# Performance work log

Measured on AMD Instinct MI355X. Metric: run time of the kernel, lower is better.

Reference implementation:

```python
import jax, jax.numpy as jnp
import numpy as np

NUM_HEADS = 8
NUM_POINTS = 4


def setup_inputs() -> dict:
    key = jax.random.key(0)
    ks = jax.random.split(key, 8)
    B, N, C, H, W = 8, 8192, 256, 128, 128
    HP2 = NUM_HEADS * NUM_POINTS * 2
    HP = NUM_HEADS * NUM_POINTS
    query = jax.random.normal(ks[0], (B, N, C), jnp.float32)
    reference_points = jax.random.uniform(ks[1], (B, N, 2), dtype=jnp.float32)
    value = jax.random.normal(ks[2], (B, C, H, W), jnp.float32)
    # learned params (offset gen is zero-init in the original; use small random
    W_off = jax.random.normal(ks[3], (C, HP2), jnp.float32) * 0.02
    b_off = jnp.zeros((HP2,), jnp.float32)
    W_attn = jax.random.normal(ks[4], (C, HP), jnp.float32) * (1.0 / np.sqrt(C))
    b_attn = jnp.zeros((HP,), jnp.float32)
    W_out = jax.random.normal(ks[5], (C, C), jnp.float32) * (1.0 / np.sqrt(C))
    b_out = jnp.zeros((C,), jnp.float32)
    return dict(query=query, reference_points=reference_points, value=value,
                W_off=W_off, b_off=b_off, W_attn=W_attn, b_attn=b_attn,
                W_out=W_out, b_out=b_out, H=H, W=W)


def reference(query, reference_points, value, W_off, b_off, W_attn, b_attn,
              W_out, b_out, H, W):
    B, N, C = query.shape
    Hh, P = NUM_HEADS, NUM_POINTS
    D = C // Hh

    offset = (query @ W_off + b_off).reshape(B, N, Hh, P, 2)
    attn = jax.nn.softmax((query @ W_attn + b_attn).reshape(B, N, Hh, P), axis=-1)

    # sampling locations in grid_sample convention: (x, y) in [-1, 1]
    ref = reference_points * 2.0 - 1.0
    loc = ref[:, :, None, None, :] + offset  # (B, N, Hh, P, 2)

    # value -> (B, Hh, H*W, D)
    val = value.reshape(B, Hh, D, H, W).transpose(0, 1, 3, 4, 2).reshape(B, Hh, H * W, D)

    # align_corners=False pixel coordinates
    x = (loc[..., 0] + 1.0) * (W * 0.5) - 0.5  # (B, N, Hh, P)
    y = (loc[..., 1] + 1.0) * (H * 0.5) - 0.5
    x0f = jnp.floor(x); y0f = jnp.floor(y)
    wx1 = x - x0f; wy1 = y - y0f
    x0 = x0f.astype(jnp.int32); y0 = y0f.astype(jnp.int32)
    x1 = x0 + 1; y1 = y0 + 1

    def gather(ix, iy, w):
        # bilinear corner gather with zero padding (mask out-of-bounds)
        valid = (ix >= 0) & (ix < W) & (iy >= 0) & (iy < H)
        idx = jnp.clip(iy, 0, H - 1) * W + jnp.clip(ix, 0, W - 1)  # (B,N,Hh,P)
        idx_t = idx.transpose(0, 2, 1, 3).reshape(B, Hh, N * P)
        g = jnp.take_along_axis(val, idx_t[..., None], axis=2)  # (B,Hh,N*P,D)
        g = g.reshape(B, Hh, N, P, D).transpose(0, 2, 1, 3, 4)  # (B,N,Hh,P,D)
        return g * (w * valid)[..., None]

    sampled = (gather(x0, y0, (1 - wx1) * (1 - wy1))
               + gather(x1, y0, wx1 * (1 - wy1))
               + gather(x0, y1, (1 - wx1) * wy1)
               + gather(x1, y1, wx1 * wy1))  # (B,N,Hh,P,D)

    out = jnp.einsum('bnhk,bnhkd->bnhd', attn, sampled).reshape(B, N, C)
    return out @ W_out + b_out
```

## Files before the change

kernel.cpp:

```cpp
#include <hip/hip_runtime.h>
#include <hip/hip_bf16.h>
#include <hip/hip_fp16.h>
#include <cstddef>

#define B_  8
#define N_  8192
#define C_  256
#define H_  128
#define W_  128
#define HH  8
#define PP  4
#define DD  32
#define HW  (H_ * W_)

typedef short bf16x8 __attribute__((ext_vector_type(8)));
typedef _Float16 f16x8 __attribute__((ext_vector_type(8)));
typedef float f32x4  __attribute__((ext_vector_type(4)));

static __device__ __forceinline__ short f2bf_s(float f) {
    __hip_bfloat16 b = __float2bfloat16(f);
    return *reinterpret_cast<short*>(&b);
}
static __device__ __forceinline__ float bf_s2f(short s) {
    __hip_bfloat16 b = *reinterpret_cast<__hip_bfloat16*>(&s);
    return __bfloat162float(b);
}

__global__ __launch_bounds__(256) void kTP(const float* __restrict__ value,
                                           __half* __restrict__ val,
                                           const float* __restrict__ W_off,
                                           const float* __restrict__ W_attn,
                                           short* __restrict__ Wc_hi,
                                           short* __restrict__ Wc_lo,
                                           const float* __restrict__ Wsrc,
                                           __half* __restrict__ Wt) {
    __shared__ __align__(16) char smem[33280];
    const int t   = threadIdx.x;
    const int bid = blockIdx.x;

    if (bid < 4096) {
        float* tf = (float*)smem;
        const int bh   = bid >> 6;
        const int pix0 = (bid & 63) * 256;
        const float* src = value + (size_t)bh * 32 * HW + pix0;
#pragma unroll
        for (int i = 0; i < 8; ++i) {
            int d = i * 4 + (t >> 6);
            int s = t & 63;
            float4 v = *(const float4*)&src[(size_t)d * HW + s * 4];
            int sx = s ^ ((d >> 3) << 2);
            *(float4*)&tf[d * 260 + sx * 4] = v;
        }
        __syncthreads();
        const int u  = t >> 2;
        const int a  = t & 3;
        const int d0 = a * 8;
#pragma unroll
        for (int j = 0; j < 4; ++j) {
            int pix = j * 64 + u;
            short o[8];
#pragma unroll
            for (int k = 0; k < 8; ++k) {
                int row = d0 + k;
                float f = tf[row * 260 +
                             (((pix >> 2) ^ (a << 2)) << 2) + (pix & 3)];
                __half hh = __float2half(f);
                o[k] = *reinterpret_cast<short*>(&hh);
            }
            *(bf16x8*)&val[((size_t)bh * HW + pix0 + pix) * 32 + d0] =
                *(bf16x8*)o;
        }
    } else if (bid < 4192) {
        const int c = bid - 4096;
        float v = (c < 64) ? W_off[(size_t)t * 64 + c]
                           : W_attn[(size_t)t * 32 + (c - 64)];
        short h = f2bf_s(v);
        short l = f2bf_s(v - bf_s2f(h));
        Wc_hi[(size_t)c * 256 + t] = h;
        Wc_lo[(size_t)c * 256 + t] = l;
    } else {
        float (*tile)[65] = (float (*)[65])smem;
        const int bx = bid - 4192;
        const int n0 = (bx & 3) * 64;
        const int k0 = (bx >> 2) * 64;
#pragma unroll
        for (int i = 0; i < 16; ++i) {
            int kk = i * 4 + (t >> 6);
            int nn = t & 63;
            tile[kk][nn] = Wsrc[(size_t)(k0 + kk) * 256 + n0 + nn];
        }
        __syncthreads();
#pragma unroll
        for (int i = 0; i < 16; ++i) {
            int nn = i * 4 + (t >> 6);
            int kk = t & 63;
            Wt[(size_t)(n0 + nn) * 256 + k0 + kk] = __float2half(tile[kk][nn]);
        }
    }
}

__global__ __launch_bounds__(256) void kA1M(const float* __restrict__ query,
                                            const float* __restrict__ refp,
                                            const short* __restrict__ Wc_hi,
                                            const short* __restrict__ Wc_lo,
                                            const float* __restrict__ b_off,
                                            const float* __restrict__ b_attn,
                                            float4* __restrict__ locattn) {
    __shared__ __align__(16) char smem[57344];
    short* As_hi = (short*)smem;
    short* As_lo = (short*)(smem + 16384);
    short* Bs_hi = (short*)(smem + 32768);
    short* Bs_lo = (short*)(smem + 45056);
    float* Ct    = (float*)smem;

    const int t    = threadIdx.x;
    const int lane = t & 63;
    const int w    = t >> 6;
    const int wm   = (w & 1) * 64;
    const int wn   = (w >> 1) * 48;
    const int quad = lane >> 4;
    const int l16  = lane & 15;
    const int row0 = blockIdx.x * 128;

    f32x4 acc[4][3];
#pragma unroll
    for (int mt = 0; mt < 4; ++mt)
#pragma unroll
        for (int nt = 0; nt < 3; ++nt)
            acc[mt][nt] = (f32x4){0.f, 0.f, 0.f, 0.f};

    for (int k0c = 0; k0c < 4; ++k0c) {
#pragma unroll
        for (int i = 0; i < 8; ++i) {
            int f   = t + i * 256;
            int row = f >> 4;
            int kq4 = f & 15;
            float4 q = *(const float4*)&query[(size_t)(row0 + row) * 256 +
                                              k0c * 64 + kq4 * 4];
            short4 hv, lv;
            hv.x = f2bf_s(q.x); lv.x = f2bf_s(q.x - bf_s2f(hv.x));
            hv.y = f2bf_s(q.y); lv.y = f2bf_s(q.y - bf_s2f(hv.y));
            hv.z = f2bf_s(q.z); lv.z = f2bf_s(q.z - bf_s2f(hv.z));
            hv.w = f2bf_s(q.w); lv.w = f2bf_s(q.w - bf_s2f(hv.w));
            int base = row * 64 + (((kq4 >> 1) ^ (row & 7)) * 8) + (kq4 & 1) * 4;
            *(short4*)&As_hi[base] = hv;
            *(short4*)&As_lo[base] = lv;
        }
#pragma unroll
        for (int i = 0; i < 3; ++i) {
            int idx = t + i * 256;
            int n   = idx >> 3;
            int kb  = idx & 7;
            int dst = n * 64 + ((kb ^ (n & 7)) * 8);
            *(uint4*)&Bs_hi[dst] =
                *(const uint4*)&Wc_hi[(size_t)n * 256 + k0c * 64 + kb * 8];
            *(uint4*)&Bs_lo[dst] =
                *(const uint4*)&Wc_lo[(size_t)n * 256 + k0c * 64 + kb * 8];
        }
        __syncthreads();

#pragma unroll
        for (int ks = 0; ks < 2; ++ks) {
            const int kq = ks * 4 + quad;
            bf16x8 ah[4], al[4], bh[3], bl[3];
#pragma unroll
            for (int mt = 0; mt < 4; ++mt) {
                int m = wm + mt * 16 + l16;
                ah[mt] = *(const bf16x8*)&As_hi[m * 64 + (kq ^ (m & 7)) * 8];
                al[mt] = *(const bf16x8*)&As_lo[m * 64 + (kq ^ (m & 7)) * 8];
            }
#pragma unroll
            for (int nt = 0; nt < 3; ++nt) {
                int n = wn + nt * 16 + l16;
                bh[nt] = *(const bf16x8*)&Bs_hi[n * 64 + (kq ^ (n & 7)) * 8];
                bl[nt] = *(const bf16x8*)&Bs_lo[n * 64 + (kq ^ (n & 7)) * 8];
            }
#pragma unroll
            for (int mt = 0; mt < 4; ++mt)
#pragma unroll
                for (int nt = 0; nt < 3; ++nt)
                    acc[mt][nt] = __builtin_amdgcn_mfma_f32_16x16x32_bf16(
                        ah[mt], bh[nt], acc[mt][nt], 0, 0, 0);
#pragma unroll
            for (int mt = 0; mt < 4; ++mt)
#pragma unroll
                for (int nt = 0; nt < 3; ++nt)
                    acc[mt][nt] = __builtin_amdgcn_mfma_f32_16x16x32_bf16(
                        ah[mt], bl[nt], acc[mt][nt], 0, 0, 0);
#pragma unroll
            for (int mt = 0; mt < 4; ++mt)
#pragma unroll
                for (int nt = 0; nt < 3; ++nt)
                    acc[mt][nt] = __builtin_amdgcn_mfma_f32_16x16x32_bf16(
                        al[mt], bh[nt], acc[mt][nt], 0, 0, 0);
        }
        __syncthreads();
    }

#pragma unroll
    for (int mt = 0; mt < 4; ++mt) {
#pragma unroll
        for (int nt = 0; nt < 3; ++nt) {
            int col = wn + nt * 16 + l16;
#pragma unroll
            for (int rI = 0; rI < 4; ++rI) {
                int row = wm + mt * 16 + quad * 4 + rI;
                Ct[row * 100 + col] = acc[mt][nt][rI];
            }
        }
    }
    __syncthreads();

    const int rg = t >> 3;
    const int h  = t & 7;
    float boff[8];
#pragma unroll
    for (int j = 0; j < 8; ++j) boff[j] = b_off[h * 8 + j];
    float batn[4];
#pragma unroll
    for (int j = 0; j < 4; ++j) batn[j] = b_attn[h * 4 + j];

#pragma unroll
    for (int r = 0; r < 4; ++r) {
        int row  = rg * 4 + r;
        int rowg = row0 + row;
        float rx = refp[(size_t)rowg * 2 + 0];
        float ry = refp[(size_t)rowg * 2 + 1];
        float4 lg4 = *(const float4*)&Ct[row * 100 + 64 + h * 4];
        float lg[4] = {lg4.x + batn[0], lg4.y + batn[1],
                       lg4.z + batn[2], lg4.w + batn[3]};
        float m = fmaxf(fmaxf(lg[0], lg[1]), fmaxf(lg[2], lg[3]));
        float e[4];
        float s = 0.f;
#pragma unroll
        for (int p = 0; p < 4; ++p) { e[p] = __expf(lg[p] - m); s += e[p]; }
        float inv = 1.f / s;
        float4 o0 = *(const float4*)&Ct[row * 100 + h * 8];
        float4 o1 = *(const float4*)&Ct[row * 100 + h * 8 + 4];
        float ox[4] = {o0.x + boff[0], o0.z + boff[2],
                       o1.x + boff[4], o1.z + boff[6]};
        float oy[4] = {o0.y + boff[1], o0.w + boff[3],
                       o1.y + boff[5], o1.w + boff[7]};
#pragma unroll
        for (int p = 0; p < 4; ++p) {
            float x = (rx * 2.f + ox[p]) * (W_ * 0.5f) - 0.5f;
            float y = (ry * 2.f + oy[p]) * (H_ * 0.5f) - 0.5f;
            locattn[(size_t)rowg * 32 + h * 4 + p] =
                make_float4(x, y, e[p] * inv, 0.f);
        }
    }
}

__global__ __launch_bounds__(256, 4) void kAC(const float4* __restrict__ locattn,
                                              const __half* __restrict__ val,
                                              const __half* __restrict__ Wt,
                                              const float* __restrict__ bias,
                                              float* __restrict__ out) {
    __shared__ __align__(16) char smem[32768];
    char*  midc = smem;
    uint4* ow   = (uint4*)(smem + 16384);
    short* Bs   = (short*)(smem + 16384);

    const int t   = threadIdx.x;
    const int bid = blockIdx.x;
    const int b   = bid & 7;
    const int n0  = (bid >> 3) * 32;

#pragma unroll
    for (int i = 0; i < 4; ++i) {
        int item = t + i * 256;
        int r  = item >> 5;
        int hp = item & 31;
        float4 L = locattn[((size_t)b * N_ + n0 + r) * 32 + hp];
        float x = L.x, y = L.y, a = L.z;
        float xf = floorf(x), yf = floorf(y);
        int x0 = (int)xf, y0 = (int)yf;
        int x1 = x0 + 1, y1 = y0 + 1;
        float wx1 = x - xf, wy1 = y - yf;
        float wx0 = 1.f - wx1, wy0 = 1.f - wy1;
        int cx0 = min(max(x0, 0), W_ - 1);
        int cx1 = min(max(x1, 0), W_ - 1);
        int cy0 = min(max(y0, 0), H_ - 1);
        int cy1 = min(max(y1, 0), H_ - 1);
        bool bx0 = (x0 >= 0) & (x0 < W_);
        bool bx1 = (x1 >= 0) & (x1 < W_);
        bool by0 = (y0 >= 0) & (y0 < H_);
        bool by1 = (y1 >= 0) & (y1 < H_);
        float f00 = a * wx0 * wy0 * ((bx0 & by0) ? 1.f : 0.f);
        float f10 = a * wx1 * wy0 * ((bx1 & by0) ? 1.f : 0.f);
        float f01 = a * wx0 * wy1 * ((bx0 & by1) ? 1.f : 0.f);
        float f11 = a * wx1 * wy1 * ((bx1 & by1) ? 1.f : 0.f);
        uint4 rec;
        rec.x = (unsigned)(cy0 * W_ + cx0) | ((unsigned)(cy0 * W_ + cx1) << 16);
        rec.y = (unsigned)(cy1 * W_ + cx0) | ((unsigned)(cy1 * W_ + cx1) << 16);
        __half2 wA = __floats2half2_rn(f00, f10);
        __half2 wB = __floats2half2_rn(f01, f11);
        rec.z = *reinterpret_cast<unsigned*>(&wA);
        rec.w = *reinterpret_cast<unsigned*>(&wB);
        ow[r * 32 + (hp ^ (r & 7))] = rec;
    }
    __syncthreads();

    {
        const int j8 = t & 7;
        const int g  = t >> 3;
        const int d8 = j8 * 4;
#pragma unroll
        for (int q = 0; q < 8; ++q) {
            const char* vb = (const char*)val +
                (((size_t)b * 8 + q) * HW * 32 + d8) * 2;
            __half2 a01 = __float2half2_rn(0.f);
            __half2 a23 = __float2half2_rn(0.f);
#pragma unroll
            for (int p = 0; p < 4; ++p) {
                uint4 rec = ow[g * 32 + ((q * 4 + p) ^ (g & 7))];
                int i0 = rec.x & 0xffff, i1 = rec.x >> 16;
                int i2 = rec.y & 0xffff, i3 = rec.y >> 16;
                __half2 wA = *reinterpret_cast<__half2*>(&rec.z);
                __half2 wB = *reinterpret_cast<__half2*>(&rec.w);
                uint2 u0 = *(const uint2*)(vb + (size_t)i0 * 64);
                uint2 u1 = *(const uint2*)(vb + (size_t)i1 * 64);
                uint2 u2 = *(const uint2*)(vb + (size_t)i2 * 64);
                uint2 u3 = *(const uint2*)(vb + (size_t)i3 * 64);
                __half2 w00 = __low2half2(wA);
                a01 = __hfma2(*reinterpret_cast<__half2*>(&u0.x), w00, a01);
                a23 = __hfma2(*reinterpret_cast<__half2*>(&u0.y), w00, a23);
                __half2 w10 = __high2half2(wA);
                a01 = __hfma2(*reinterpret_cast<__half2*>(&u1.x), w10, a01);
                a23 = __hfma2(*reinterpret_cast<__half2*>(&u1.y), w10, a23);
                __half2 w01 = __low2half2(wB);
                a01 = __hfma2(*reinterpret_cast<__half2*>(&u2.x), w01, a01);
                a23 = __hfma2(*reinterpret_cast<__half2*>(&u2.y), w01, a23);
                __half2 w11 = __high2half2(wB);
                a01 = __hfma2(*reinterpret_cast<__half2*>(&u3.x), w11, a01);
                a23 = __hfma2(*reinterpret_cast<__half2*>(&u3.y), w11, a23);
            }
            int c8  = q * 4 + (j8 >> 1);
            int off = g * 512 + ((c8 ^ (g & 7)) * 16) + (j8 & 1) * 8;
            uint2 st;
            st.x = *reinterpret_cast<unsigned*>(&a01);
            st.y = *reinterpret_cast<unsigned*>(&a23);
            *(uint2*)(midc + off) = st;
        }
    }
    __syncthreads();

    const int lane = t & 63;
    const int w    = t >> 6;
    const int wn   = w * 64;
    const int quad = lane >> 4;
    const int l16  = lane & 15;

    f32x4 acc[2][4];
#pragma unroll
    for (int mt = 0; mt < 2; ++mt)
#pragma unroll
        for (int nt = 0; nt < 4; ++nt)
            acc[mt][nt] = (f32x4){0.f, 0.f, 0.f, 0.f};

    for (int k0 = 0; k0 < 8; ++k0) {
#pragma unroll
        for (int i = 0; i < 4; ++i) {
            int idx = t + i * 256;
            int n   = idx >> 2;
            int kb  = idx & 3;
            *(uint4*)&Bs[n * 32 + ((kb ^ (n & 3)) * 8)] =
                *(const uint4*)&Wt[(size_t)n * 256 + k0 * 32 + kb * 8];
        }
        __syncthreads();

        f16x8 af[2], bfv[4];
#pragma unroll
        for (int mt = 0; mt < 2; ++mt) {
            int m = mt * 16 + l16;
            af[mt] = *(const f16x8*)(midc + m * 512 +
                                     (((k0 * 4 + quad) ^ (m & 7)) * 16));
        }
#pragma unroll
        for (int nt = 0; nt < 4; ++nt) {
            int n = wn + nt * 16 + l16;
            bfv[nt] = *(const f16x8*)&Bs[n * 32 + ((quad ^ (n & 3)) * 8)];
        }
#pragma unroll
        for (int mt = 0; mt < 2; ++mt)
#pragma unroll
            for (int nt = 0; nt < 4; ++nt)
                acc[mt][nt] = __builtin_amdgcn_mfma_f32_16x16x32_f16(
                    af[mt], bfv[nt], acc[mt][nt], 0, 0, 0);
        __syncthreads();
    }

    float* ost = (float*)smem;
#pragma unroll
    for (int nt = 0; nt < 4; ++nt) {
        int col  = wn + nt * 16 + l16;
        float bv = bias[col];
#pragma unroll
        for (int mt = 0; mt < 2; ++mt) {
#pragma unroll
            for (int rI = 0; rI < 4; ++rI) {
                int row = mt * 16 + quad * 4 + rI;
                int byt = row * 1024 + ((col * 4) ^ ((row & 1) << 6));
                *(float*)((char*)ost + byt) = acc[mt][nt][rI] + bv;
            }
        }
    }
    __syncthreads();
#pragma unroll
    for (int i = 0; i < 8; ++i) {
        int idx = t + i * 256;
        int row = idx >> 6;
        int u   = idx & 63;
        float4 v = *(const float4*)((char*)ost +
                                    row * 1024 + ((u * 16) ^ ((row & 1) << 6)));
        *(float4*)&out[((size_t)b * N_ + n0 + row) * 256 + u * 4] = v;
    }
}

extern "C" void kernel_launch(void* const* d_in, const int* in_sizes, int n_in,
                              void* d_out, int out_size, void* d_ws, size_t ws_size,
                              hipStream_t stream) {
    const float* query  = (const float*)d_in[0];
    const float* refp   = (const float*)d_in[1];
    const float* value  = (const float*)d_in[2];
    const float* W_off  = (const float*)d_in[3];
    const float* b_off  = (const float*)d_in[4];
    const float* W_attn = (const float*)d_in[5];
    const float* b_attn = (const float*)d_in[6];
    const float* W_out  = (const float*)d_in[7];
    const float* b_out  = (const float*)d_in[8];
    float* out = (float*)d_out;

    char*   ws      = (char*)d_ws;
    __half* val     = (__half*)(ws);
    float4* locattn = (float4*)(ws + 67108864);
    __half* Wt      = (__half*)(ws + 134217728);
    short*  Wc_hi   = (short*)(ws + 134348800);
    short*  Wc_lo   = (short*)(ws + 134397952);

    kTP <<<dim3(4208), 256, 0, stream>>>(value, val, W_off, W_attn,
                                         Wc_hi, Wc_lo, W_out, Wt);
    kA1M<<<dim3((B_ * N_) / 128), 256, 0, stream>>>(query, refp, Wc_hi, Wc_lo,
                                                    b_off, b_attn, locattn);
    kAC <<<dim3((B_ * N_) / 32), 256, 0, stream>>>(locattn, val, Wt,
                                                   b_out, out);
}
```

Baseline: 364.0 us.

## Co-schedule value transpose with offset GEMM in one launch, raise kAC occupancy

The value-to-fp16 transpose blocks move out of the prep kernel into the offset/attention GEMM kernel as extra blocks, so the bandwidth-bound transpose can overlap with the compute-bound GEMM. A small prep kernel keeps only the weight conversions, and it must finish before the GEMM blocks that read its output. kAC launch bounds go from 4 to 5 waves per SIMD, which may force register spills. The transpose blocks now also reserve the larger 57KB shared allocation, which can limit how many fit per CU.

Measured after the change: 356.9 us. About the same (-2.0%).

```diff
diff --git a/kernel.cpp b/kernel.cpp
--- a/kernel.cpp
+++ b/kernel.cpp
@@ -26,52 +26,16 @@
     return __bfloat162float(b);
 }
 
-__global__ __launch_bounds__(256) void kTP(const float* __restrict__ value,
-                                           __half* __restrict__ val,
-                                           const float* __restrict__ W_off,
-                                           const float* __restrict__ W_attn,
-                                           short* __restrict__ Wc_hi,
-                                           short* __restrict__ Wc_lo,
-                                           const float* __restrict__ Wsrc,
-                                           __half* __restrict__ Wt) {
-    __shared__ __align__(16) char smem[33280];
-    const int t   = threadIdx.x;
-    const int bid = blockIdx.x;
-
-    if (bid < 4096) {
-        float* tf = (float*)smem;
-        const int bh   = bid >> 6;
-        const int pix0 = (bid & 63) * 256;
-        const float* src = value + (size_t)bh * 32 * HW + pix0;
-#pragma unroll
-        for (int i = 0; i < 8; ++i) {
-            int d = i * 4 + (t >> 6);
-            int s = t & 63;
-            float4 v = *(const float4*)&src[(size_t)d * HW + s * 4];
-            int sx = s ^ ((d >> 3) << 2);
-            *(float4*)&tf[d * 260 + sx * 4] = v;
-        }
-        __syncthreads();
-        const int u  = t >> 2;
-        const int a  = t & 3;
-        const int d0 = a * 8;
-#pragma unroll
-        for (int j = 0; j < 4; ++j) {
-            int pix = j * 64 + u;
-            short o[8];
-#pragma unroll
-            for (int k = 0; k < 8; ++k) {
-                int row = d0 + k;
-                float f = tf[row * 260 +
-                             (((pix >> 2) ^ (a << 2)) << 2) + (pix & 3)];
-                __half hh = __float2half(f);
-                o[k] = *reinterpret_cast<short*>(&hh);
-            }
-            *(bf16x8*)&val[((size_t)bh * HW + pix0 + pix) * 32 + d0] =
-                *(bf16x8*)o;
-        }
-    } else if (bid < 4192) {
-        const int c = bid - 4096;
+__global__ __launch_bounds__(256) void kP(const float* __restrict__ W_off,
+                                          const float* __restrict__ W_attn,
+                                          short* __restrict__ Wc_hi,
+                                          short* __restrict__ Wc_lo,
+                                          const float* __restrict__ Wsrc,
+                                          __half* __restrict__ Wt) {
+    __shared__ float tile[64][65];
+    const int t = threadIdx.x;
+    if (blockIdx.x < 96) {
+        const int c = blockIdx.x;
         float v = (c < 64) ? W_off[(size_t)t * 64 + c]
                            : W_attn[(size_t)t * 32 + (c - 64)];
         short h = f2bf_s(v);
@@ -79,8 +43,7 @@
         Wc_hi[(size_t)c * 256 + t] = h;
         Wc_lo[(size_t)c * 256 + t] = l;
     } else {
-        float (*tile)[65] = (float (*)[65])smem;
-        const int bx = bid - 4192;
+        const int bx = blockIdx.x - 96;
         const int n0 = (bx & 3) * 64;
         const int k0 = (bx >> 2) * 64;
 #pragma unroll
@@ -99,28 +62,68 @@
     }
 }
 
-__global__ __launch_bounds__(256) void kA1M(const float* __restrict__ query,
-                                            const float* __restrict__ refp,
-                                            const short* __restrict__ Wc_hi,
-                                            const short* __restrict__ Wc_lo,
-                                            const float* __restrict__ b_off,
-                                            const float* __restrict__ b_attn,
-                                            float4* __restrict__ locattn) {
+__global__ __launch_bounds__(256) void kMain(const float* __restrict__ query,
+                                             const float* __restrict__ refp,
+                                             const short* __restrict__ Wc_hi,
+                                             const short* __restrict__ Wc_lo,
+                                             const float* __restrict__ b_off,
+                                             const float* __restrict__ b_attn,
+                                             float4* __restrict__ locattn,
+                                             const float* __restrict__ value,
+                                             __half* __restrict__ val) {
     __shared__ __align__(16) char smem[57344];
+    const int t   = threadIdx.x;
+    const int bid = blockIdx.x;
+
+    if (bid >= 512) {
+        float* tf = (float*)smem;
+        const int tb   = bid - 512;
+        const int bh   = tb >> 6;
+        const int pix0 = (tb & 63) * 256;
+        const float* src = value + (size_t)bh * 32 * HW + pix0;
+#pragma unroll
+        for (int i = 0; i < 8; ++i) {
+            int d = i * 4 + (t >> 6);
+            int s = t & 63;
+            float4 v = *(const float4*)&src[(size_t)d * HW + s * 4];
+            int sx = s ^ ((d >> 3) << 2);
+            *(float4*)&tf[d * 260 + sx * 4] = v;
+        }
+        __syncthreads();
+        const int u  = t >> 2;
+        const int a  = t & 3;
+        const int d0 = a * 8;
+#pragma unroll
+        for (int j = 0; j < 4; ++j) {
+            int pix = j * 64 + u;
+            short o[8];
+#pragma unroll
+            for (int k = 0; k < 8; ++k) {
+                int row = d0 + k;
+                float f = tf[row * 260 +
+                             (((pix >> 2) ^ (a << 2)) << 2) + (pix & 3)];
+                __half hh = __float2half(f);
+                o[k] = *reinterpret_cast<short*>(&hh);
+            }
+            *(bf16x8*)&val[((size_t)bh * HW + pix0 + pix) * 32 + d0] =
+                *(bf16x8*)o;
+        }
+        return;
+    }
+
     short* As_hi = (short*)smem;
     short* As_lo = (short*)(smem + 16384);
     short* Bs_hi = (short*)(smem + 32768);
     short* Bs_lo = (short*)(smem + 45056);
     float* Ct    = (float*)smem;
 
-    const int t    = threadIdx.x;
     const int lane = t & 63;
     const int w    = t >> 6;
     const int wm   = (w & 1) * 64;
     const int wn   = (w >> 1) * 48;
     const int quad = lane >> 4;
     const int l16  = lane & 15;
-    const int row0 = blockIdx.x * 128;
+    const int row0 = bid * 128;
 
     f32x4 acc[4][3];
 #pragma unroll
@@ -251,7 +254,7 @@
     }
 }
 
-__global__ __launch_bounds__(256, 4) void kAC(const float4* __restrict__ locattn,
+__global__ __launch_bounds__(256, 5) void kAC(const float4* __restrict__ locattn,
                                               const __half* __restrict__ val,
                                               const __half* __restrict__ Wt,
                                               const float* __restrict__ bias,
@@ -438,10 +441,10 @@
     short*  Wc_hi   = (short*)(ws + 134348800);
     short*  Wc_lo   = (short*)(ws + 134397952);
 
-    kTP <<<dim3(4208), 256, 0, stream>>>(value, val, W_off, W_attn,
-                                         Wc_hi, Wc_lo, W_out, Wt);
-    kA1M<<<dim3((B_ * N_) / 128), 256, 0, stream>>>(query, refp, Wc_hi, Wc_lo,
-                                                    b_off, b_attn, locattn);
-    kAC <<<dim3((B_ * N_) / 32), 256, 0, stream>>>(locattn, val, Wt,
-                                                   b_out, out);
-}
+    kP   <<<dim3(112), 256, 0, stream>>>(W_off, W_attn, Wc_hi, Wc_lo,
+                                         W_out, Wt);
+    kMain<<<dim3(4608), 256, 0, stream>>>(query, refp, Wc_hi, Wc_lo,
+                                          b_off, b_attn, locattn, value, val);
+    kAC  <<<dim3((B_ * N_) / 32), 256, 0, stream>>>(locattn, val, Wt,
+                                                    b_out, out);
+}
```
